# Kernel tuning notes

Measured on AMD Instinct MI355X. Metric: run time of the kernel, lower is better.

The kernel has to match this reference:

```python
import jax, jax.numpy as jnp
import numpy as np

B, N, C, NH = 8, 16384, 256, 8
CH = C // NH          # head dim = 32
SCALE = CH ** -0.5
HH = WW = 128         # N = HH*WW
# CoaT crpe window dict {3:2, 5:3, 7:3}: 2 heads->3x3, 3 heads->5x5, 3 heads->7x7


def setup_inputs() -> dict:
    key = jax.random.key(0)
    ks = jax.random.split(key, 9)
    w = lambda k, shp: (jax.random.normal(k, shp, jnp.float32) * 0.02)
    return {
        "x": jax.random.normal(ks[0], (B, N, C), jnp.float32),
        "w_qkv": w(ks[1], (C, 3 * C)),              # qkv_bias=False
        "w_proj": w(ks[2], (C, C)),
        "b_proj": jnp.zeros((C,), jnp.float32),
        "w3": w(ks[3], (3, 3, 1, 2 * CH)),          # HWIO depthwise, 2 heads
        "b3": jnp.zeros((2 * CH,), jnp.float32),
        "w5": w(ks[4], (5, 5, 1, 3 * CH)),          # 3 heads
        "b5": jnp.zeros((3 * CH,), jnp.float32),
        "w7": w(ks[5], (7, 7, 1, 3 * CH)),          # 3 heads
        "b7": jnp.zeros((3 * CH,), jnp.float32),
        "H": HH,
        "W": WW,
    }


def _hydra(q, k, v):
    # q,k,v: [B, h, N, Ch]; normalize over feature dim, O(N) token reduction
    qn = q * jax.lax.rsqrt(jnp.sum(q * q, axis=-1, keepdims=True))
    kn = k * jax.lax.rsqrt(jnp.sum(k * k, axis=-1, keepdims=True))
    kv = jnp.sum(kn * v, axis=-2, keepdims=True)   # [B, h, 1, Ch]
    return qn * kv                                  # broadcast over tokens


def _dwconv(img, kern, bias):
    # img: [B, c, H, W]; kern: [kh, kw, 1, c] (HWIO depthwise)
    c = img.shape[1]
    out = jax.lax.conv_general_dilated(
        img, kern, window_strides=(1, 1), padding="SAME",
        feature_group_count=c,
        dimension_numbers=("NCHW", "HWIO", "NCHW"))
    return out + bias[None, :, None, None]


def _crpe(q, v, Hs, Ws, convs):
    # CoaT ConvRelPosEnc: depthwise conv on v per head group, gated by q
    b, h, n, ch = v.shape
    outs, idx = [], 0
    for heads, kern, bias in convs:
        vs = v[:, idx:idx + heads]                          # [B, hs, N, Ch]
        v_img = vs.transpose(0, 1, 3, 2).reshape(b, heads * ch, Hs, Ws)
        cv = _dwconv(v_img, kern, bias)
        cv = cv.reshape(b, heads, ch, n).transpose(0, 1, 3, 2)
        outs.append(q[:, idx:idx + heads] * cv)
        idx += heads
    return jnp.concatenate(outs, axis=1)                    # [B, h, N, Ch]


def reference(x, w_qkv, w_proj, b_proj, w3, b3, w5, b5, w7, b7, H, W):
    b, n, c = x.shape
    qkv = (x @ w_qkv).reshape(b, n, 3, NH, CH).transpose(2, 0, 3, 1, 4)
    q, k, v = qkv[0], qkv[1], qkv[2]                        # [B, h, N, Ch]
    factor_att = _hydra(q, k, v)
    crpe = _crpe(q, v, H, W, [(2, w3, b3), (3, w5, b5), (3, w7, b7)])
    out = SCALE * factor_att + crpe
    out = out.transpose(0, 2, 1, 3).reshape(b, n, c)        # [B, N, C]
    return out @ w_proj + b_proj
```

## Files before the change

kernel.cpp:

```cpp
#include <hip/hip_runtime.h>
#include <hip/hip_bf16.h>


typedef __hip_bfloat16 bf16;
typedef __bf16 bf16x8 __attribute__((ext_vector_type(8)));
typedef unsigned short u16x8 __attribute__((ext_vector_type(8)));
typedef float f32x4 __attribute__((ext_vector_type(4)));
typedef float f32x8 __attribute__((ext_vector_type(8)));

#define SCALE_ 0.17677669529663687f

__device__ __forceinline__ unsigned short f2b(float f) {
  __hip_bfloat16 h = __float2bfloat16(f);
  return __builtin_bit_cast(unsigned short, h);
}
__device__ __forceinline__ float blo(unsigned u) {
  return __builtin_bit_cast(float, u << 16);
}
__device__ __forceinline__ float bhi(unsigned u) {
  return __builtin_bit_cast(float, u & 0xffff0000u);
}
__device__ __forceinline__ f32x8 unpack8(uint4 u) {
  f32x8 r;
  r[0] = blo(u.x); r[1] = bhi(u.x); r[2] = blo(u.y); r[3] = bhi(u.y);
  r[4] = blo(u.z); r[5] = bhi(u.z); r[6] = blo(u.w); r[7] = bhi(u.w);
  return r;
}
__device__ __forceinline__ uint4 pack8(float a0, float a1, float a2, float a3,
                                       float a4, float a5, float a6, float a7) {
  uint4 s;
  s.x = (unsigned)f2b(a0) | ((unsigned)f2b(a1) << 16);
  s.y = (unsigned)f2b(a2) | ((unsigned)f2b(a3) << 16);
  s.z = (unsigned)f2b(a4) | ((unsigned)f2b(a5) << 16);
  s.w = (unsigned)f2b(a6) | ((unsigned)f2b(a7) << 16);
  return s;
}
__device__ __forceinline__ void gload16(const void* g, void* l) {
  __builtin_amdgcn_global_load_lds(
      (const __attribute__((address_space(1))) unsigned int*)g,
      (__attribute__((address_space(3))) unsigned int*)l, 16, 0, 0);
}
__device__ __forceinline__ f32x4 mfma16(u16x8 a, u16x8 b, f32x4 c) {
  return __builtin_amdgcn_mfma_f32_16x16x32_bf16(
      __builtin_bit_cast(bf16x8, a), __builtin_bit_cast(bf16x8, b), c, 0, 0, 0);
}

__global__ __launch_bounds__(256) void prep_weights(
    const float* __restrict__ wqkv, const float* __restrict__ wproj,
    bf16* __restrict__ wqkvT, bf16* __restrict__ wprojT) {
  const int idx = blockIdx.x * 256 + threadIdx.x;
  if (idx < 768 * 256) {
    const int j = idx >> 8, k = idx & 255;
    wqkvT[idx] = __float2bfloat16(wqkv[k * 768 + j]);
  }
  if (idx < 256 * 256) {
    const int j = idx >> 8, k = idx & 255;
    wprojT[idx] = __float2bfloat16(wproj[k * 256 + j]);
  }
}

__global__ __launch_bounds__(256) void qkv_mfma(
    const float* __restrict__ x, const bf16* __restrict__ wT,
    bf16* __restrict__ qO, bf16* __restrict__ kO, bf16* __restrict__ vO) {
  __shared__ __align__(16) char LDSU[32768];
  char* As = LDSU;
  char* Bs = LDSU + 16384;
  const int tid = threadIdx.x;
  const int l = tid & 63, w = tid >> 6;
  const int wr = w >> 1, wc = w & 1;

  const int lin = blockIdx.y * 6 + blockIdx.x;
  const int xcd = lin & 7, qq = lin >> 3;
  const int jt = qq % 6;
  const int ttile = xcd * 128 + qq / 6;
  const int j0 = jt << 7;
  const int t0 = ttile << 7;

  f32x4 acc[4][4];
#pragma unroll
  for (int m = 0; m < 4; ++m)
#pragma unroll
    for (int t = 0; t < 4; ++t) acc[m][t] = (f32x4){0.f, 0.f, 0.f, 0.f};

  const int arow0 = w * 16 + (l >> 2), arow1 = arow0 + 64;
  const int asl = l & 3;
  const bf16* asrc0 =
      wT + (size_t)(j0 + arow0) * 256 + ((asl ^ ((arow0 >> 1) & 3)) << 3);
  const bf16* asrc1 =
      wT + (size_t)(j0 + arow1) * 256 + ((asl ^ ((arow1 >> 1) & 3)) << 3);
  const int ad0 = w * 1024;
  const int ad1 = 4096 + w * 1024;

  const int brow = tid >> 1, bkh = tid & 1;
  const float* xp = x + (size_t)(t0 + brow) * 256 + bkh * 16;
  const int bsw = (brow >> 1) & 3;
  const int bw0 = brow * 64 + (((bkh << 1) ^ bsw) << 4);
  const int bw1 = brow * 64 + ((((bkh << 1) | 1) ^ bsw) << 4);

  const int fr = l & 15;
  const int fq = l >> 4;
  const int fs = (fq ^ ((l >> 1) & 3)) << 4;

  {
    const float4 xa0 = *(const float4*)(xp);
    const float4 xa1 = *(const float4*)(xp + 4);
    const float4 xa2 = *(const float4*)(xp + 8);
    const float4 xa3 = *(const float4*)(xp + 12);
    gload16(asrc0, As + ad0);
    gload16(asrc1, As + ad1);
    u16x8 p0, p1;
    p0[0] = f2b(xa0.x); p0[1] = f2b(xa0.y); p0[2] = f2b(xa0.z); p0[3] = f2b(xa0.w);
    p0[4] = f2b(xa1.x); p0[5] = f2b(xa1.y); p0[6] = f2b(xa1.z); p0[7] = f2b(xa1.w);
    p1[0] = f2b(xa2.x); p1[1] = f2b(xa2.y); p1[2] = f2b(xa2.z); p1[3] = f2b(xa2.w);
    p1[4] = f2b(xa3.x); p1[5] = f2b(xa3.y); p1[6] = f2b(xa3.z); p1[7] = f2b(xa3.w);
    *(u16x8*)(Bs + bw0) = p0;
    *(u16x8*)(Bs + bw1) = p1;
  }
  __syncthreads();

  int cur = 0;
  for (int t = 0; t < 8; ++t) {
    const int kn = (t + 1) << 5;
    const int nxt = (cur ^ 1) << 13;
    float4 xa0, xa1, xa2, xa3;
    if (t < 7) {
      xa0 = *(const float4*)(xp + kn);
      xa1 = *(const float4*)(xp + kn + 4);
      xa2 = *(const float4*)(xp + kn + 8);
      xa3 = *(const float4*)(xp + kn + 12);
      gload16(asrc0 + kn, As + nxt + ad0);
      gload16(asrc1 + kn, As + nxt + ad1);
    }
    const char* Ac = As + (cur << 13);
    const char* Bc = Bs + (cur << 13);
    u16x8 af[4], bfv[4];
#pragma unroll
    for (int m = 0; m < 4; ++m)
      af[m] = *(const u16x8*)(Ac + (wr * 64 + m * 16 + fr) * 64 + fs);
#pragma unroll
    for (int tt = 0; tt < 4; ++tt)
      bfv[tt] = *(const u16x8*)(Bc + (wc * 64 + tt * 16 + fr) * 64 + fs);
#pragma unroll
    for (int m = 0; m < 4; ++m)
#pragma unroll
      for (int tt = 0; tt < 4; ++tt)
        acc[m][tt] = mfma16(af[m], bfv[tt], acc[m][tt]);
    if (t < 7) {
      u16x8 p0, p1;
      p0[0] = f2b(xa0.x); p0[1] = f2b(xa0.y); p0[2] = f2b(xa0.z); p0[3] = f2b(xa0.w);
      p0[4] = f2b(xa1.x); p0[5] = f2b(xa1.y); p0[6] = f2b(xa1.z); p0[7] = f2b(xa1.w);
      p1[0] = f2b(xa2.x); p1[1] = f2b(xa2.y); p1[2] = f2b(xa2.z); p1[3] = f2b(xa2.w);
      p1[4] = f2b(xa3.x); p1[5] = f2b(xa3.y); p1[6] = f2b(xa3.z); p1[7] = f2b(xa3.w);
      *(u16x8*)(Bs + nxt + bw0) = p0;
      *(u16x8*)(Bs + nxt + bw1) = p1;
    }
    __syncthreads();
    cur ^= 1;
  }

#pragma unroll
  for (int m = 0; m < 4; ++m) {
    const int jq = wr * 16 + m * 4 + fq;
#pragma unroll
    for (int t = 0; t < 4; ++t) {
      const int token = wc * 64 + t * 16 + fr;
      const int p = jq ^ (token & 15);
      uint2 pk;
      pk.x = (unsigned)f2b(acc[m][t][0]) | ((unsigned)f2b(acc[m][t][1]) << 16);
      pk.y = (unsigned)f2b(acc[m][t][2]) | ((unsigned)f2b(acc[m][t][3]) << 16);
      *(uint2*)(LDSU + token * 256 + (p << 3)) = pk;
    }
  }
  __syncthreads();

  const int region = j0 >> 8;
  bf16* outp = (region == 0) ? qO : ((region == 1) ? kO : vO);
  const int b = t0 >> 14;
  const int n0 = t0 & 16383;
  const int jl = j0 & 255;
  const int seg = tid & 15;
#pragma unroll
  for (int r = 0; r < 8; ++r) {
    const int token = r * 16 + (tid >> 4);
    const int tsw = token & 15;
    const int q0 = (2 * seg) ^ tsw;
    const int q1 = (2 * seg + 1) ^ tsw;
    const uint2 lo = *(const uint2*)(LDSU + token * 256 + (q0 << 3));
    const uint2 hi = *(const uint2*)(LDSU + token * 256 + (q1 << 3));
    uint4 d;
    d.x = lo.x; d.y = lo.y; d.z = hi.x; d.w = hi.y;
    *(uint4*)&outp[((size_t)b * 16384 + n0 + token) * 256 + jl + seg * 8] = d;
  }
}

__global__ __launch_bounds__(256) void kv_reduce(
    const bf16* __restrict__ kT, const bf16* __restrict__ vT,
    float* __restrict__ kv) {
  __shared__ float red[256 * 8];
  const int tid = threadIdx.x;
  const int b = blockIdx.y;
  const int seg = tid & 31;
  f32x8 part = (f32x8)0.f;

  for (int r = 0; r < 32; ++r) {
    const int token = blockIdx.x * 256 + r * 8 + (tid >> 5);
    const size_t roff = ((size_t)b * 16384 + token) * 256;
    const uint4 kd = *(const uint4*)(kT + roff + seg * 8);
    const f32x8 kf = unpack8(kd);
    float ss = 0.f;
#pragma unroll
    for (int i = 0; i < 8; ++i) ss += kf[i] * kf[i];
    ss += __shfl_xor(ss, 1);
    ss += __shfl_xor(ss, 2);
    const float inv = rsqrtf(ss);
    const uint4 vd = *(const uint4*)(vT + roff + seg * 8);
    const f32x8 vf = unpack8(vd);
#pragma unroll
    for (int i = 0; i < 8; ++i) part[i] += kf[i] * inv * vf[i];
  }
#pragma unroll
  for (int i = 0; i < 8; ++i) red[tid * 8 + i] = part[i];
  __syncthreads();
  if (tid < 32) {
    f32x8 s = (f32x8)0.f;
#pragma unroll
    for (int k = 0; k < 8; ++k)
#pragma unroll
      for (int i = 0; i < 8; ++i) s[i] += red[(tid + 32 * k) * 8 + i];
#pragma unroll
    for (int i = 0; i < 8; ++i)
      atomicAdd(&kv[b * 256 + seg * 8 + i], s[i]);
  }
}

template <int K>
__global__ __launch_bounds__(256) void crpe_conv(
    const bf16* __restrict__ qT, const bf16* __restrict__ vT,
    const float* __restrict__ kvbuf, const float* __restrict__ wp,
    const float* __restrict__ bp, int OC, int hbase,
    bf16* __restrict__ mid) {
  constexpr int R = K / 2;
  constexpr int S = 16 + 2 * R;
  constexpr int NSLOT = 4 * ((S - 1) * 23 + 1);
  __shared__ __align__(16) char vs[NSLOT * 16];
  __shared__ float wlds[K * K * 32];
  __shared__ float blds[32];

  const int tid = threadIdx.x;
  const int hg = blockIdx.x;
  const int h = hbase + hg;
  const int tile = blockIdx.y;
  const int b = blockIdx.z;
  const int tx0 = (tile & 7) * 16, ty0 = (tile >> 3) * 16;
  const int px = tid & 15, py = tid >> 4;
  const int ocbase = hg * 32;

  for (int e = tid; e < S * S; e += 256) {
    const int ly = e / S, lx = e - ly * S;
    const int gy = ty0 - R + ly, gx = tx0 - R + lx;
    uint4 d0 = {0, 0, 0, 0}, d1 = {0, 0, 0, 0}, d2 = {0, 0, 0, 0},
          d3 = {0, 0, 0, 0};
    if (gy >= 0 && gy < 128 && gx >= 0 && gx < 128) {
      const uint4* src = (const uint4*)(vT +
          ((size_t)b * 16384 + gy * 128 + gx) * 256 + h * 32);
      d0 = src[0]; d1 = src[1]; d2 = src[2]; d3 = src[3];
    }
    const int p = ly * 22 + lx;
    const int sw = (p >> 1) & 3;
    char* base = vs + ((p << 2) << 4);
    *(uint4*)(base + ((0 ^ sw) << 4)) = d0;
    *(uint4*)(base + ((1 ^ sw) << 4)) = d1;
    *(uint4*)(base + ((2 ^ sw) << 4)) = d2;
    *(uint4*)(base + ((3 ^ sw) << 4)) = d3;
  }
  for (int e = tid; e < K * K * 32; e += 256)
    wlds[e] = wp[(e >> 5) * OC + ocbase + (e & 31)];
  if (tid < 32) blds[tid] = bp[ocbase + tid];
  __syncthreads();

  const float4* bl4 = (const float4*)blds;
  f32x8 acc[4];
#pragma unroll
  for (int cc = 0; cc < 4; ++cc) {
    const float4 b0 = bl4[cc * 2], b1 = bl4[cc * 2 + 1];
    acc[cc][0] = b0.x; acc[cc][1] = b0.y; acc[cc][2] = b0.z; acc[cc][3] = b0.w;
    acc[cc][4] = b1.x; acc[cc][5] = b1.y; acc[cc][6] = b1.z; acc[cc][7] = b1.w;
  }
  const float4* wlds4 = (const float4*)wlds;
#pragma unroll 1
  for (int ky = 0; ky < K; ++ky) {
#pragma unroll
    for (int kx = 0; kx < K; ++kx) {
      const int p = (py + ky) * 22 + (px + kx);
      const int tap = ky * K + kx;
      const int sw = (p >> 1) & 3;
      const char* base = vs + ((p << 2) << 4);
#pragma unroll
      for (int cc = 0; cc < 4; ++cc) {
        const uint4 vv = *(const uint4*)(base + ((cc ^ sw) << 4));
        const f32x8 vf = unpack8(vv);
        const float4 w0 = wlds4[tap * 8 + cc * 2];
        const float4 w1 = wlds4[tap * 8 + cc * 2 + 1];
        acc[cc][0] += vf[0] * w0.x; acc[cc][1] += vf[1] * w0.y;
        acc[cc][2] += vf[2] * w0.z; acc[cc][3] += vf[3] * w0.w;
        acc[cc][4] += vf[4] * w1.x; acc[cc][5] += vf[5] * w1.y;
        acc[cc][6] += vf[6] * w1.z; acc[cc][7] += vf[7] * w1.w;
      }
    }
  }

  const int n = (ty0 + py) * 128 + (tx0 + px);
  const size_t off = ((size_t)b * 16384 + n) * 256 + h * 32;
  const uint4* qsrc = (const uint4*)(qT + off);
  f32x8 qv[4];
  float ss = 0.f;
#pragma unroll
  for (int cc = 0; cc < 4; ++cc) {
    qv[cc] = unpack8(qsrc[cc]);
#pragma unroll
    for (int i = 0; i < 8; ++i) ss += qv[cc][i] * qv[cc][i];
  }
  const float qinv = rsqrtf(ss);
  const float4* kvp = (const float4*)(kvbuf + ((size_t)b * 8 + h) * 32);
  uint4* mdst = (uint4*)(mid + off);
#pragma unroll
  for (int cc = 0; cc < 4; ++cc) {
    const float4 ka = kvp[cc * 2], kb = kvp[cc * 2 + 1];
    float o[8];
    o[0] = SCALE_ * qv[cc][0] * qinv * ka.x + qv[cc][0] * acc[cc][0];
    o[1] = SCALE_ * qv[cc][1] * qinv * ka.y + qv[cc][1] * acc[cc][1];
    o[2] = SCALE_ * qv[cc][2] * qinv * ka.z + qv[cc][2] * acc[cc][2];
    o[3] = SCALE_ * qv[cc][3] * qinv * ka.w + qv[cc][3] * acc[cc][3];
    o[4] = SCALE_ * qv[cc][4] * qinv * kb.x + qv[cc][4] * acc[cc][4];
    o[5] = SCALE_ * qv[cc][5] * qinv * kb.y + qv[cc][5] * acc[cc][5];
    o[6] = SCALE_ * qv[cc][6] * qinv * kb.z + qv[cc][6] * acc[cc][6];
    o[7] = SCALE_ * qv[cc][7] * qinv * kb.w + qv[cc][7] * acc[cc][7];
    mdst[cc] = pack8(o[0], o[1], o[2], o[3], o[4], o[5], o[6], o[7]);
  }
}

__global__ __launch_bounds__(256) void proj_mfma(
    const bf16* __restrict__ mid, const bf16* __restrict__ wpT,
    const float* __restrict__ bproj, float* __restrict__ out) {
  __shared__ __align__(16) char LDSU[32768];
  char* As = LDSU;
  char* Bs = LDSU + 16384;
  const int tid = threadIdx.x;
  const int l = tid & 63, w = tid >> 6;
  const int wr = w >> 1, wc = w & 1;

  const int lin = blockIdx.y * 2 + blockIdx.x;
  const int xcd = lin & 7, qq = lin >> 3;
  const int jt = qq & 1;
  const int ttile = xcd * 128 + (qq >> 1);
  const int j0 = jt << 7;
  const int tk0 = ttile << 7;

  f32x4 acc[4][4];
#pragma unroll
  for (int m = 0; m < 4; ++m)
#pragma unroll
    for (int t = 0; t < 4; ++t) acc[m][t] = (f32x4){0.f, 0.f, 0.f, 0.f};

  const int row0 = w * 16 + (l >> 2), row1 = row0 + 64;
  const int sl = l & 3;
  const int sw0 = (row0 >> 1) & 3, sw1 = (row1 >> 1) & 3;
  const bf16* asrc0 = wpT + (size_t)(j0 + row0) * 256 + ((sl ^ sw0) << 3);
  const bf16* asrc1 = wpT + (size_t)(j0 + row1) * 256 + ((sl ^ sw1) << 3);
  const bf16* bsrc0 = mid + (size_t)(tk0 + row0) * 256 + ((sl ^ sw0) << 3);
  const bf16* bsrc1 = mid + (size_t)(tk0 + row1) * 256 + ((sl ^ sw1) << 3);
  const int d0 = w * 1024;
  const int d1 = 4096 + w * 1024;

  const int fr = l & 15;
  const int fq = l >> 4;
  const int fs = (fq ^ ((l >> 1) & 3)) << 4;

  gload16(asrc0, As + d0);
  gload16(asrc1, As + d1);
  gload16(bsrc0, Bs + d0);
  gload16(bsrc1, Bs + d1);
  __syncthreads();

  int cur = 0;
  for (int t = 0; t < 8; ++t) {
    const int kn = (t + 1) << 5;
    const int nxt = (cur ^ 1) << 13;
    if (t < 7) {
      gload16(asrc0 + kn, As + nxt + d0);
      gload16(asrc1 + kn, As + nxt + d1);
      gload16(bsrc0 + kn, Bs + nxt + d0);
      gload16(bsrc1 + kn, Bs + nxt + d1);
    }
    const char* Ac = As + (cur << 13);
    const char* Bc = Bs + (cur << 13);
    u16x8 af[4], bfv[4];
#pragma unroll
    for (int m = 0; m < 4; ++m)
      af[m] = *(const u16x8*)(Ac + (wr * 64 + m * 16 + fr) * 64 + fs);
#pragma unroll
    for (int tt = 0; tt < 4; ++tt)
      bfv[tt] = *(const u16x8*)(Bc + (wc * 64 + tt * 16 + fr) * 64 + fs);
#pragma unroll
    for (int m = 0; m < 4; ++m)
#pragma unroll
      for (int tt = 0; tt < 4; ++tt)
        acc[m][tt] = mfma16(af[m], bfv[tt], acc[m][tt]);
    __syncthreads();
    cur ^= 1;
  }

#pragma unroll
  for (int m = 0; m < 4; ++m) {
    const float4 bias = *(const float4*)&bproj[j0 + wr * 64 + m * 16 + fq * 4];
#pragma unroll
    for (int t = 0; t < 4; ++t) {
      acc[m][t][0] += bias.x;
      acc[m][t][1] += bias.y;
      acc[m][t][2] += bias.z;
      acc[m][t][3] += bias.w;
    }
  }

  for (int chunk = 0; chunk < 2; ++chunk) {
    if (wc == chunk) {
#pragma unroll
      for (int m = 0; m < 4; ++m) {
        const int jq = wr * 16 + m * 4 + fq;
#pragma unroll
        for (int t = 0; t < 4; ++t) {
          const int ltok = t * 16 + fr;
          const int p = jq ^ (ltok & 15);
          float4 r;
          r.x = acc[m][t][0]; r.y = acc[m][t][1];
          r.z = acc[m][t][2]; r.w = acc[m][t][3];
          *(float4*)(LDSU + ltok * 512 + (p << 4)) = r;
        }
      }
    }
    __syncthreads();
    const int seg = tid & 31;
#pragma unroll
    for (int r = 0; r < 8; ++r) {
      const int ltok = r * 8 + (tid >> 5);
      const int p = seg ^ (ltok & 15);
      const float4 dv = *(const float4*)(LDSU + ltok * 512 + (p << 4));
      *(float4*)&out[(size_t)(tk0 + chunk * 64 + ltok) * 256 + j0 + seg * 4] = dv;
    }
    __syncthreads();
  }
}

extern "C" void kernel_launch(void* const* d_in, const int* in_sizes, int n_in,
                              void* d_out, int out_size, void* d_ws,
                              size_t ws_size, hipStream_t stream) {
  const float* x     = (const float*)d_in[0];
  const float* wqkv  = (const float*)d_in[1];
  const float* wproj = (const float*)d_in[2];
  const float* bproj = (const float*)d_in[3];
  const float* w3 = (const float*)d_in[4];
  const float* b3 = (const float*)d_in[5];
  const float* w5 = (const float*)d_in[6];
  const float* b5 = (const float*)d_in[7];
  const float* w7 = (const float*)d_in[8];
  const float* b7 = (const float*)d_in[9];
  float* out = (float*)d_out;

  const size_t PLANE = (size_t)8 * 16384 * 256;
  bf16* qT  = (bf16*)d_ws;
  bf16* vT  = qT + PLANE;
  bf16* kT  = vT + PLANE;
  bf16* mid = kT;
  float* kv = (float*)(kT + PLANE);
  bf16* wqkvT  = (bf16*)(kv + 2048);
  bf16* wprojT = wqkvT + 768 * 256;

  hipMemsetAsync(kv, 0, 2048 * sizeof(float), stream);
  prep_weights<<<dim3(768), 256, 0, stream>>>(wqkv, wproj, wqkvT, wprojT);
  qkv_mfma<<<dim3(6, 1024), 256, 0, stream>>>(x, wqkvT, qT, kT, vT);
  kv_reduce<<<dim3(64, 8), 256, 0, stream>>>(kT, vT, kv);
  crpe_conv<3><<<dim3(2, 64, 8), 256, 0, stream>>>(qT, vT, kv, w3, b3, 64, 0, mid);
  crpe_conv<5><<<dim3(3, 64, 8), 256, 0, stream>>>(qT, vT, kv, w5, b5, 96, 2, mid);
  crpe_conv<7><<<dim3(3, 64, 8), 256, 0, stream>>>(qT, vT, kv, w7, b7, 96, 5, mid);
  proj_mfma<<<dim3(2, 1024), 256, 0, stream>>>(mid, wprojT, bproj, out);
}
```

Measured before the change: 344.8 us.

## Keep full token tile resident in LDS and loop over all output column tiles

Both GEMM kernels now load a 128-token × 256 K activation tile once into LDS (converting x to bf16 in qkv) and loop over all output column tiles inside one block, streaming only the weight slices. This removes the 6× (qkv) and 2× (proj) re-reads and re-conversions of the activation rows across separate blocks. In exchange, each block uses 80 KB LDS, which lowers occupancy. The grid shrinks to 1024 blocks and the column loop runs serially, with extra syncs per tile.

```diff
diff --git a/kernel.cpp b/kernel.cpp
--- a/kernel.cpp
+++ b/kernel.cpp
@@ -62,134 +62,122 @@
 __global__ __launch_bounds__(256) void qkv_mfma(
     const float* __restrict__ x, const bf16* __restrict__ wT,
     bf16* __restrict__ qO, bf16* __restrict__ kO, bf16* __restrict__ vO) {
-  __shared__ __align__(16) char LDSU[32768];
-  char* As = LDSU;
-  char* Bs = LDSU + 16384;
+  __shared__ __align__(16) char XL[65536];
+  __shared__ __align__(16) char WB[16384];
   const int tid = threadIdx.x;
   const int l = tid & 63, w = tid >> 6;
   const int wr = w >> 1, wc = w & 1;
-
-  const int lin = blockIdx.y * 6 + blockIdx.x;
-  const int xcd = lin & 7, qq = lin >> 3;
-  const int jt = qq % 6;
-  const int ttile = xcd * 128 + qq / 6;
-  const int j0 = jt << 7;
-  const int t0 = ttile << 7;
-
-  f32x4 acc[4][4];
-#pragma unroll
-  for (int m = 0; m < 4; ++m)
-#pragma unroll
-    for (int t = 0; t < 4; ++t) acc[m][t] = (f32x4){0.f, 0.f, 0.f, 0.f};
+  const int t0 = (int)blockIdx.x << 7;
+  const int b = t0 >> 14;
+  const int n0 = t0 & 16383;
+
+  {
+    const int tk = tid >> 5;
+    const int s = tid & 31;
+    for (int r = 0; r < 16; ++r) {
+      const int row = r * 8 + tk;
+      const float4 a0 = *(const float4*)(x + (size_t)(t0 + row) * 256 + s * 8);
+      const float4 a1 =
+          *(const float4*)(x + (size_t)(t0 + row) * 256 + s * 8 + 4);
+      u16x8 p;
+      p[0] = f2b(a0.x); p[1] = f2b(a0.y); p[2] = f2b(a0.z); p[3] = f2b(a0.w);
+      p[4] = f2b(a1.x); p[5] = f2b(a1.y); p[6] = f2b(a1.z); p[7] = f2b(a1.w);
+      *(u16x8*)(XL + row * 512 + ((s ^ (row & 7)) << 4)) = p;
+    }
+  }
 
   const int arow0 = w * 16 + (l >> 2), arow1 = arow0 + 64;
   const int asl = l & 3;
-  const bf16* asrc0 =
-      wT + (size_t)(j0 + arow0) * 256 + ((asl ^ ((arow0 >> 1) & 3)) << 3);
-  const bf16* asrc1 =
-      wT + (size_t)(j0 + arow1) * 256 + ((asl ^ ((arow1 >> 1) & 3)) << 3);
-  const int ad0 = w * 1024;
-  const int ad1 = 4096 + w * 1024;
-
-  const int brow = tid >> 1, bkh = tid & 1;
-  const float* xp = x + (size_t)(t0 + brow) * 256 + bkh * 16;
-  const int bsw = (brow >> 1) & 3;
-  const int bw0 = brow * 64 + (((bkh << 1) ^ bsw) << 4);
-  const int bw1 = brow * 64 + ((((bkh << 1) | 1) ^ bsw) << 4);
+  const int aoff0 = ((asl ^ ((arow0 >> 1) & 3)) << 3);
+  const int aoff1 = ((asl ^ ((arow1 >> 1) & 3)) << 3);
+  const int ad0 = w * 1024, ad1 = 4096 + w * 1024;
 
   const int fr = l & 15;
   const int fq = l >> 4;
   const int fs = (fq ^ ((l >> 1) & 3)) << 4;
 
-  {
-    const float4 xa0 = *(const float4*)(xp);
-    const float4 xa1 = *(const float4*)(xp + 4);
-    const float4 xa2 = *(const float4*)(xp + 8);
-    const float4 xa3 = *(const float4*)(xp + 12);
-    gload16(asrc0, As + ad0);
-    gload16(asrc1, As + ad1);
-    u16x8 p0, p1;
-    p0[0] = f2b(xa0.x); p0[1] = f2b(xa0.y); p0[2] = f2b(xa0.z); p0[3] = f2b(xa0.w);
-    p0[4] = f2b(xa1.x); p0[5] = f2b(xa1.y); p0[6] = f2b(xa1.z); p0[7] = f2b(xa1.w);
-    p1[0] = f2b(xa2.x); p1[1] = f2b(xa2.y); p1[2] = f2b(xa2.z); p1[3] = f2b(xa2.w);
-    p1[4] = f2b(xa3.x); p1[5] = f2b(xa3.y); p1[6] = f2b(xa3.z); p1[7] = f2b(xa3.w);
-    *(u16x8*)(Bs + bw0) = p0;
-    *(u16x8*)(Bs + bw1) = p1;
-  }
-  __syncthreads();
-
-  int cur = 0;
-  for (int t = 0; t < 8; ++t) {
-    const int kn = (t + 1) << 5;
-    const int nxt = (cur ^ 1) << 13;
-    float4 xa0, xa1, xa2, xa3;
-    if (t < 7) {
-      xa0 = *(const float4*)(xp + kn);
-      xa1 = *(const float4*)(xp + kn + 4);
-      xa2 = *(const float4*)(xp + kn + 8);
-      xa3 = *(const float4*)(xp + kn + 12);
-      gload16(asrc0 + kn, As + nxt + ad0);
-      gload16(asrc1 + kn, As + nxt + ad1);
-    }
-    const char* Ac = As + (cur << 13);
-    const char* Bc = Bs + (cur << 13);
-    u16x8 af[4], bfv[4];
+  int btok[4], btsw[4];
+#pragma unroll
+  for (int tt = 0; tt < 4; ++tt) {
+    btok[tt] = wc * 64 + tt * 16 + fr;
+    btsw[tt] = btok[tt] & 7;
+  }
+
+#pragma unroll 1
+  for (int jt = 0; jt < 6; ++jt) {
+    const bf16* wbase = wT + (size_t)jt * 128 * 256;
+    f32x4 acc[4][4];
 #pragma unroll
     for (int m = 0; m < 4; ++m)
-      af[m] = *(const u16x8*)(Ac + (wr * 64 + m * 16 + fr) * 64 + fs);
-#pragma unroll
-    for (int tt = 0; tt < 4; ++tt)
-      bfv[tt] = *(const u16x8*)(Bc + (wc * 64 + tt * 16 + fr) * 64 + fs);
-#pragma unroll
-    for (int m = 0; m < 4; ++m)
+#pragma unroll
+      for (int t = 0; t < 4; ++t) acc[m][t] = (f32x4){0.f, 0.f, 0.f, 0.f};
+
+    gload16(wbase + (size_t)arow0 * 256 + aoff0, WB + ad0);
+    gload16(wbase + (size_t)arow1 * 256 + aoff1, WB + ad1);
+
+#pragma unroll 1
+    for (int t = 0; t < 8; ++t) {
+      __syncthreads();
+      if (t < 7) {
+        const int kn = (t + 1) * 32;
+        const int nb = ((t + 1) & 1) << 13;
+        gload16(wbase + (size_t)arow0 * 256 + kn + aoff0, WB + nb + ad0);
+        gload16(wbase + (size_t)arow1 * 256 + kn + aoff1, WB + nb + ad1);
+      }
+      const char* Ac = WB + ((t & 1) << 13);
+      u16x8 af[4], bfv[4];
+#pragma unroll
+      for (int m = 0; m < 4; ++m)
+        af[m] = *(const u16x8*)(Ac + (wr * 64 + m * 16 + fr) * 64 + fs);
 #pragma unroll
       for (int tt = 0; tt < 4; ++tt)
-        acc[m][tt] = mfma16(af[m], bfv[tt], acc[m][tt]);
-    if (t < 7) {
-      u16x8 p0, p1;
-      p0[0] = f2b(xa0.x); p0[1] = f2b(xa0.y); p0[2] = f2b(xa0.z); p0[3] = f2b(xa0.w);
-      p0[4] = f2b(xa1.x); p0[5] = f2b(xa1.y); p0[6] = f2b(xa1.z); p0[7] = f2b(xa1.w);
-      p1[0] = f2b(xa2.x); p1[1] = f2b(xa2.y); p1[2] = f2b(xa2.z); p1[3] = f2b(xa2.w);
-      p1[4] = f2b(xa3.x); p1[5] = f2b(xa3.y); p1[6] = f2b(xa3.z); p1[7] = f2b(xa3.w);
-      *(u16x8*)(Bs + nxt + bw0) = p0;
-      *(u16x8*)(Bs + nxt + bw1) = p1;
-    }
+        bfv[tt] = *(const u16x8*)(XL + btok[tt] * 512 +
+                                  (((4 * t + fq) ^ btsw[tt]) << 4));
+#pragma unroll
+      for (int m = 0; m < 4; ++m)
+#pragma unroll
+        for (int tt = 0; tt < 4; ++tt)
+          acc[m][tt] = mfma16(af[m], bfv[tt], acc[m][tt]);
+    }
+
+    const int region = jt >> 1;
+    bf16* outp = (region == 0) ? qO : ((region == 1) ? kO : vO);
+    const int jl = (jt & 1) * 128;
     __syncthreads();
-    cur ^= 1;
-  }
-
-#pragma unroll
-  for (int m = 0; m < 4; ++m) {
-    const int jq = wr * 16 + m * 4 + fq;
-#pragma unroll
-    for (int t = 0; t < 4; ++t) {
-      const int token = wc * 64 + t * 16 + fr;
-      const int p = jq ^ (token & 15);
-      uint2 pk;
-      pk.x = (unsigned)f2b(acc[m][t][0]) | ((unsigned)f2b(acc[m][t][1]) << 16);
-      pk.y = (unsigned)f2b(acc[m][t][2]) | ((unsigned)f2b(acc[m][t][3]) << 16);
-      *(uint2*)(LDSU + token * 256 + (p << 3)) = pk;
-    }
-  }
-  __syncthreads();
-
-  const int region = j0 >> 8;
-  bf16* outp = (region == 0) ? qO : ((region == 1) ? kO : vO);
-  const int b = t0 >> 14;
-  const int n0 = t0 & 16383;
-  const int jl = j0 & 255;
-  const int seg = tid & 15;
-#pragma unroll
-  for (int r = 0; r < 8; ++r) {
-    const int token = r * 16 + (tid >> 4);
-    const int tsw = token & 15;
-    const int q0 = (2 * seg) ^ tsw;
-    const int q1 = (2 * seg + 1) ^ tsw;
-    const uint2 lo = *(const uint2*)(LDSU + token * 256 + (q0 << 3));
-    const uint2 hi = *(const uint2*)(LDSU + token * 256 + (q1 << 3));
-    uint4 d;
-    d.x = lo.x; d.y = lo.y; d.z = hi.x; d.w = hi.y;
-    *(uint4*)&outp[((size_t)b * 16384 + n0 + token) * 256 + jl + seg * 8] = d;
+#pragma unroll 1
+    for (int c = 0; c < 2; ++c) {
+      if (wc == c) {
+#pragma unroll
+        for (int m = 0; m < 4; ++m) {
+          const int jq = wr * 16 + m * 4 + fq;
+#pragma unroll
+          for (int tt = 0; tt < 4; ++tt) {
+            const int ltok = tt * 16 + fr;
+            uint2 pk;
+            pk.x = (unsigned)f2b(acc[m][tt][0]) |
+                   ((unsigned)f2b(acc[m][tt][1]) << 16);
+            pk.y = (unsigned)f2b(acc[m][tt][2]) |
+                   ((unsigned)f2b(acc[m][tt][3]) << 16);
+            *(uint2*)(WB + ltok * 256 + ((jq ^ (ltok & 15)) << 3)) = pk;
+          }
+        }
+      }
+      __syncthreads();
+      const int seg = tid & 15;
+#pragma unroll
+      for (int r = 0; r < 4; ++r) {
+        const int ltok = r * 16 + (tid >> 4);
+        const int tsw = ltok & 15;
+        const uint2 lo = *(const uint2*)(WB + ltok * 256 + (((2 * seg) ^ tsw) << 3));
+        const uint2 hi =
+            *(const uint2*)(WB + ltok * 256 + (((2 * seg + 1) ^ tsw) << 3));
+        uint4 d;
+        d.x = lo.x; d.y = lo.y; d.z = hi.x; d.w = hi.y;
+        *(uint4*)&outp[((size_t)b * 16384 + n0 + c * 64 + ltok) * 256 + jl +
+                       seg * 8] = d;
+      }
+      __syncthreads();
+    }
   }
 }
 
@@ -342,112 +330,132 @@
 __global__ __launch_bounds__(256) void proj_mfma(
     const bf16* __restrict__ mid, const bf16* __restrict__ wpT,
     const float* __restrict__ bproj, float* __restrict__ out) {
-  __shared__ __align__(16) char LDSU[32768];
-  char* As = LDSU;
-  char* Bs = LDSU + 16384;
+  __shared__ __align__(16) char XL[65536];
+  __shared__ __align__(16) char WB[16384];
   const int tid = threadIdx.x;
   const int l = tid & 63, w = tid >> 6;
   const int wr = w >> 1, wc = w & 1;
-
-  const int lin = blockIdx.y * 2 + blockIdx.x;
-  const int xcd = lin & 7, qq = lin >> 3;
-  const int jt = qq & 1;
-  const int ttile = xcd * 128 + (qq >> 1);
-  const int j0 = jt << 7;
-  const int tk0 = ttile << 7;
-
-  f32x4 acc[4][4];
-#pragma unroll
-  for (int m = 0; m < 4; ++m)
-#pragma unroll
-    for (int t = 0; t < 4; ++t) acc[m][t] = (f32x4){0.f, 0.f, 0.f, 0.f};
-
-  const int row0 = w * 16 + (l >> 2), row1 = row0 + 64;
-  const int sl = l & 3;
-  const int sw0 = (row0 >> 1) & 3, sw1 = (row1 >> 1) & 3;
-  const bf16* asrc0 = wpT + (size_t)(j0 + row0) * 256 + ((sl ^ sw0) << 3);
-  const bf16* asrc1 = wpT + (size_t)(j0 + row1) * 256 + ((sl ^ sw1) << 3);
-  const bf16* bsrc0 = mid + (size_t)(tk0 + row0) * 256 + ((sl ^ sw0) << 3);
-  const bf16* bsrc1 = mid + (size_t)(tk0 + row1) * 256 + ((sl ^ sw1) << 3);
-  const int d0 = w * 1024;
-  const int d1 = 4096 + w * 1024;
+  const int t0 = (int)blockIdx.x << 7;
+  const int b = t0 >> 14;
+  const int n0 = t0 & 16383;
+
+  {
+    const int ltk = l >> 5;
+    const int s = l & 31;
+#pragma unroll 1
+    for (int i = 0; i < 16; ++i) {
+      const int shot_tok = w * 32 + i * 2;
+      const int tok = shot_tok + ltk;
+      gload16(mid + ((size_t)b * 16384 + n0 + tok) * 256 +
+                  ((s ^ (tok & 7)) << 3),
+              XL + shot_tok * 512);
+    }
+  }
+
+  const int arow0 = w * 16 + (l >> 2), arow1 = arow0 + 64;
+  const int asl = l & 3;
+  const int aoff0 = ((asl ^ ((arow0 >> 1) & 3)) << 3);
+  const int aoff1 = ((asl ^ ((arow1 >> 1) & 3)) << 3);
+  const int ad0 = w * 1024, ad1 = 4096 + w * 1024;
 
   const int fr = l & 15;
   const int fq = l >> 4;
   const int fs = (fq ^ ((l >> 1) & 3)) << 4;
 
-  gload16(asrc0, As + d0);
-  gload16(asrc1, As + d1);
-  gload16(bsrc0, Bs + d0);
-  gload16(bsrc1, Bs + d1);
-  __syncthreads();
-
-  int cur = 0;
-  for (int t = 0; t < 8; ++t) {
-    const int kn = (t + 1) << 5;
-    const int nxt = (cur ^ 1) << 13;
-    if (t < 7) {
-      gload16(asrc0 + kn, As + nxt + d0);
-      gload16(asrc1 + kn, As + nxt + d1);
-      gload16(bsrc0 + kn, Bs + nxt + d0);
-      gload16(bsrc1 + kn, Bs + nxt + d1);
-    }
-    const char* Ac = As + (cur << 13);
-    const char* Bc = Bs + (cur << 13);
-    u16x8 af[4], bfv[4];
+  int btok[4], btsw[4];
+#pragma unroll
+  for (int tt = 0; tt < 4; ++tt) {
+    btok[tt] = wc * 64 + tt * 16 + fr;
+    btsw[tt] = btok[tt] & 7;
+  }
+
+#pragma unroll 1
+  for (int jt = 0; jt < 2; ++jt) {
+    const bf16* wbase = wpT + (size_t)jt * 128 * 256;
+    const int j0 = jt * 128;
+    f32x4 acc[4][4];
 #pragma unroll
     for (int m = 0; m < 4; ++m)
-      af[m] = *(const u16x8*)(Ac + (wr * 64 + m * 16 + fr) * 64 + fs);
-#pragma unroll
-    for (int tt = 0; tt < 4; ++tt)
-      bfv[tt] = *(const u16x8*)(Bc + (wc * 64 + tt * 16 + fr) * 64 + fs);
-#pragma unroll
-    for (int m = 0; m < 4; ++m)
+#pragma unroll
+      for (int t = 0; t < 4; ++t) acc[m][t] = (f32x4){0.f, 0.f, 0.f, 0.f};
+
+    gload16(wbase + (size_t)arow0 * 256 + aoff0, WB + ad0);
+    gload16(wbase + (size_t)arow1 * 256 + aoff1, WB + ad1);
+
+#pragma unroll 1
+    for (int t = 0; t < 8; ++t) {
+      __syncthreads();
+      if (t < 7) {
+        const int kn = (t + 1) * 32;
+        const int nb = ((t + 1) & 1) << 13;
+        gload16(wbase + (size_t)arow0 * 256 + kn + aoff0, WB + nb + ad0);
+        gload16(wbase + (size_t)arow1 * 256 + kn + aoff1, WB + nb + ad1);
+      }
+      const char* Ac = WB + ((t & 1) << 13);
+      u16x8 af[4], bfv[4];
+#pragma unroll
+      for (int m = 0; m < 4; ++m)
+        af[m] = *(const u16x8*)(Ac + (wr * 64 + m * 16 + fr) * 64 + fs);
 #pragma unroll
       for (int tt = 0; tt < 4; ++tt)
-        acc[m][tt] = mfma16(af[m], bfv[tt], acc[m][tt]);
+        bfv[tt] = *(const u16x8*)(XL + btok[tt] * 512 +
+                                  (((4 * t + fq) ^ btsw[tt]) << 4));
+#pragma unroll
+      for (int m = 0; m < 4; ++m)
+#pragma unroll
+        for (int tt = 0; tt < 4; ++tt)
+          acc[m][tt] = mfma16(af[m], bfv[tt], acc[m][tt]);
+    }
+
+#pragma unroll
+    for (int m = 0; m < 4; ++m) {
+      const float4 bias =
+          *(const float4*)&bproj[j0 + wr * 64 + m * 16 + fq * 4];
+#pragma unroll
+      for (int t = 0; t < 4; ++t) {
+        acc[m][t][0] += bias.x;
+        acc[m][t][1] += bias.y;
+        acc[m][t][2] += bias.z;
+        acc[m][t][3] += bias.w;
+      }
+    }
+
     __syncthreads();
-    cur ^= 1;
-  }
-
-#pragma unroll
-  for (int m = 0; m < 4; ++m) {
-    const float4 bias = *(const float4*)&bproj[j0 + wr * 64 + m * 16 + fq * 4];
-#pragma unroll
-    for (int t = 0; t < 4; ++t) {
-      acc[m][t][0] += bias.x;
-      acc[m][t][1] += bias.y;
-      acc[m][t][2] += bias.z;
-      acc[m][t][3] += bias.w;
-    }
-  }
-
-  for (int chunk = 0; chunk < 2; ++chunk) {
-    if (wc == chunk) {
-#pragma unroll
-      for (int m = 0; m < 4; ++m) {
-        const int jq = wr * 16 + m * 4 + fq;
-#pragma unroll
-        for (int t = 0; t < 4; ++t) {
-          const int ltok = t * 16 + fr;
-          const int p = jq ^ (ltok & 15);
-          float4 r;
-          r.x = acc[m][t][0]; r.y = acc[m][t][1];
-          r.z = acc[m][t][2]; r.w = acc[m][t][3];
-          *(float4*)(LDSU + ltok * 512 + (p << 4)) = r;
+#pragma unroll 1
+    for (int r = 0; r < 4; ++r) {
+      if (wc == (r >> 1)) {
+        const int tb = (r & 1) * 2;
+#pragma unroll
+        for (int m = 0; m < 4; ++m) {
+          const int sq = wr * 16 + m * 4 + fq;
+#pragma unroll
+          for (int ti = 0; ti < 2; ++ti) {
+            const int tt = tb + ti;
+            const int ltok = ti * 16 + fr;
+            float4 rv;
+            rv.x = acc[m][tt][0]; rv.y = acc[m][tt][1];
+            rv.z = acc[m][tt][2]; rv.w = acc[m][tt][3];
+            *(float4*)(WB + ltok * 512 + ((sq ^ (ltok & 7)) << 4)) = rv;
+          }
         }
       }
-    }
-    __syncthreads();
-    const int seg = tid & 31;
-#pragma unroll
-    for (int r = 0; r < 8; ++r) {
-      const int ltok = r * 8 + (tid >> 5);
-      const int p = seg ^ (ltok & 15);
-      const float4 dv = *(const float4*)(LDSU + ltok * 512 + (p << 4));
-      *(float4*)&out[(size_t)(tk0 + chunk * 64 + ltok) * 256 + j0 + seg * 4] = dv;
-    }
-    __syncthreads();
+      __syncthreads();
+#pragma unroll
+      for (int i = 0; i < 2; ++i) {
+        const int lin = i * 256 + tid;
+        const int ltok = lin >> 5, seg = lin & 31;
+        const float4 dv =
+            *(const float4*)(WB + ltok * 512 + ((seg ^ (ltok & 7)) << 4));
+        *(float4*)&out[(size_t)(t0 + r * 32 + ltok) * 256 + j0 + seg * 4] = dv;
+        const int lin2 = lin + 512;
+        const int ltok2 = lin2 >> 5, seg2 = lin2 & 31;
+        const float4 dv2 =
+            *(const float4*)(WB + ltok2 * 512 + ((seg2 ^ (ltok2 & 7)) << 4));
+        *(float4*)&out[(size_t)(t0 + r * 32 + ltok2) * 256 + j0 + seg2 * 4] =
+            dv2;
+      }
+      __syncthreads();
+    }
   }
 }
 
@@ -477,10 +485,10 @@
 
   hipMemsetAsync(kv, 0, 2048 * sizeof(float), stream);
   prep_weights<<<dim3(768), 256, 0, stream>>>(wqkv, wproj, wqkvT, wprojT);
-  qkv_mfma<<<dim3(6, 1024), 256, 0, stream>>>(x, wqkvT, qT, kT, vT);
+  qkv_mfma<<<dim3(1024), 256, 0, stream>>>(x, wqkvT, qT, kT, vT);
   kv_reduce<<<dim3(64, 8), 256, 0, stream>>>(kT, vT, kv);
   crpe_conv<3><<<dim3(2, 64, 8), 256, 0, stream>>>(qT, vT, kv, w3, b3, 64, 0, mid);
   crpe_conv<5><<<dim3(3, 64, 8), 256, 0, stream>>>(qT, vT, kv, w5, b5, 96, 2, mid);
   crpe_conv<7><<<dim3(3, 64, 8), 256, 0, stream>>>(qT, vT, kv, w7, b7, 96, 5, mid);
-  proj_mfma<<<dim3(2, 1024), 256, 0, stream>>>(mid, wprojT, bproj, out);
-}
+  proj_mfma<<<dim3(1024), 256, 0, stream>>>(mid, wprojT, bproj, out);
+}
```

After: 487.2 us. 1.41x slower.

## Deepen GEMM prefetch pipelines with partial-wait barriers and merge crpe conv launches

Applied to the files above, without the earlier changes.

The qkv GEMM now keeps three stages of x register prefetch in flight. The proj GEMM uses a triple-buffered LDS ring with loads issued two stages ahead. In both, full __syncthreads is replaced by s_waitcnt vmcnt(N) barriers and MFMA sections are raised with s_setprio, so global loads can overlap compute instead of draining every iteration. The three crpe conv kernels become one launch that dispatches on head index, removing two launches and the tail idle between them. Costs are more registers, more LDS in proj (48KB, which may lower occupancy) and hand-counted vmcnt values that must match the exact number of outstanding loads.

```diff
diff --git a/kernel.cpp b/kernel.cpp
--- a/kernel.cpp
+++ b/kernel.cpp
@@ -43,6 +43,21 @@
 __device__ __forceinline__ f32x4 mfma16(u16x8 a, u16x8 b, f32x4 c) {
   return __builtin_amdgcn_mfma_f32_16x16x32_bf16(
       __builtin_bit_cast(bf16x8, a), __builtin_bit_cast(bf16x8, b), c, 0, 0, 0);
+}
+__device__ __forceinline__ void barrier_vm4() {
+  asm volatile("s_waitcnt vmcnt(4) lgkmcnt(0)" ::: "memory");
+  __builtin_amdgcn_s_barrier();
+  asm volatile("" ::: "memory");
+}
+__device__ __forceinline__ void barrier_vm0() {
+  asm volatile("s_waitcnt vmcnt(0) lgkmcnt(0)" ::: "memory");
+  __builtin_amdgcn_s_barrier();
+  asm volatile("" ::: "memory");
+}
+__device__ __forceinline__ void barrier_vm8() {
+  asm volatile("s_waitcnt vmcnt(8) lgkmcnt(0)" ::: "memory");
+  __builtin_amdgcn_s_barrier();
+  asm volatile("" ::: "memory");
 }
 
 __global__ __launch_bounds__(256) void prep_weights(
@@ -88,8 +103,7 @@
       wT + (size_t)(j0 + arow0) * 256 + ((asl ^ ((arow0 >> 1) & 3)) << 3);
   const bf16* asrc1 =
       wT + (size_t)(j0 + arow1) * 256 + ((asl ^ ((arow1 >> 1) & 3)) << 3);
-  const int ad0 = w * 1024;
-  const int ad1 = 4096 + w * 1024;
+  const int ad0 = w * 1024, ad1 = 4096 + w * 1024;
 
   const int brow = tid >> 1, bkh = tid & 1;
   const float* xp = x + (size_t)(t0 + brow) * 256 + bkh * 16;
@@ -101,38 +115,45 @@
   const int fq = l >> 4;
   const int fs = (fq ^ ((l >> 1) & 3)) << 4;
 
+  float4 xs[3][4];
+
+  gload16(asrc0, As + ad0);
+  gload16(asrc1, As + ad1);
+#pragma unroll
+  for (int s = 0; s < 3; ++s)
+#pragma unroll
+    for (int i = 0; i < 4; ++i)
+      xs[s][i] = *(const float4*)(xp + s * 32 + i * 4);
   {
-    const float4 xa0 = *(const float4*)(xp);
-    const float4 xa1 = *(const float4*)(xp + 4);
-    const float4 xa2 = *(const float4*)(xp + 8);
-    const float4 xa3 = *(const float4*)(xp + 12);
-    gload16(asrc0, As + ad0);
-    gload16(asrc1, As + ad1);
     u16x8 p0, p1;
-    p0[0] = f2b(xa0.x); p0[1] = f2b(xa0.y); p0[2] = f2b(xa0.z); p0[3] = f2b(xa0.w);
-    p0[4] = f2b(xa1.x); p0[5] = f2b(xa1.y); p0[6] = f2b(xa1.z); p0[7] = f2b(xa1.w);
-    p1[0] = f2b(xa2.x); p1[1] = f2b(xa2.y); p1[2] = f2b(xa2.z); p1[3] = f2b(xa2.w);
-    p1[4] = f2b(xa3.x); p1[5] = f2b(xa3.y); p1[6] = f2b(xa3.z); p1[7] = f2b(xa3.w);
+    p0[0] = f2b(xs[0][0].x); p0[1] = f2b(xs[0][0].y);
+    p0[2] = f2b(xs[0][0].z); p0[3] = f2b(xs[0][0].w);
+    p0[4] = f2b(xs[0][1].x); p0[5] = f2b(xs[0][1].y);
+    p0[6] = f2b(xs[0][1].z); p0[7] = f2b(xs[0][1].w);
+    p1[0] = f2b(xs[0][2].x); p1[1] = f2b(xs[0][2].y);
+    p1[2] = f2b(xs[0][2].z); p1[3] = f2b(xs[0][2].w);
+    p1[4] = f2b(xs[0][3].x); p1[5] = f2b(xs[0][3].y);
+    p1[6] = f2b(xs[0][3].z); p1[7] = f2b(xs[0][3].w);
     *(u16x8*)(Bs + bw0) = p0;
     *(u16x8*)(Bs + bw1) = p1;
   }
-  __syncthreads();
-
-  int cur = 0;
+  barrier_vm8();
+
+#pragma unroll
   for (int t = 0; t < 8; ++t) {
-    const int kn = (t + 1) << 5;
-    const int nxt = (cur ^ 1) << 13;
-    float4 xa0, xa1, xa2, xa3;
     if (t < 7) {
-      xa0 = *(const float4*)(xp + kn);
-      xa1 = *(const float4*)(xp + kn + 4);
-      xa2 = *(const float4*)(xp + kn + 8);
-      xa3 = *(const float4*)(xp + kn + 12);
-      gload16(asrc0 + kn, As + nxt + ad0);
-      gload16(asrc1 + kn, As + nxt + ad1);
-    }
-    const char* Ac = As + (cur << 13);
-    const char* Bc = Bs + (cur << 13);
+      const int kn = (t + 1) << 5;
+      char* Adst = As + (((t + 1) & 1) << 13);
+      gload16(asrc0 + kn, Adst + ad0);
+      gload16(asrc1 + kn, Adst + ad1);
+    }
+    if (t < 5) {
+#pragma unroll
+      for (int i = 0; i < 4; ++i)
+        xs[t % 3][i] = *(const float4*)(xp + (t + 3) * 32 + i * 4);
+    }
+    const char* Ac = As + ((t & 1) << 13);
+    const char* Bc = Bs + ((t & 1) << 13);
     u16x8 af[4], bfv[4];
 #pragma unroll
     for (int m = 0; m < 4; ++m)
@@ -140,23 +161,32 @@
 #pragma unroll
     for (int tt = 0; tt < 4; ++tt)
       bfv[tt] = *(const u16x8*)(Bc + (wc * 64 + tt * 16 + fr) * 64 + fs);
+    __builtin_amdgcn_s_setprio(1);
 #pragma unroll
     for (int m = 0; m < 4; ++m)
 #pragma unroll
       for (int tt = 0; tt < 4; ++tt)
         acc[m][tt] = mfma16(af[m], bfv[tt], acc[m][tt]);
+    __builtin_amdgcn_s_setprio(0);
     if (t < 7) {
+      const float4* xv = xs[(t + 1) % 3];
       u16x8 p0, p1;
-      p0[0] = f2b(xa0.x); p0[1] = f2b(xa0.y); p0[2] = f2b(xa0.z); p0[3] = f2b(xa0.w);
-      p0[4] = f2b(xa1.x); p0[5] = f2b(xa1.y); p0[6] = f2b(xa1.z); p0[7] = f2b(xa1.w);
-      p1[0] = f2b(xa2.x); p1[1] = f2b(xa2.y); p1[2] = f2b(xa2.z); p1[3] = f2b(xa2.w);
-      p1[4] = f2b(xa3.x); p1[5] = f2b(xa3.y); p1[6] = f2b(xa3.z); p1[7] = f2b(xa3.w);
-      *(u16x8*)(Bs + nxt + bw0) = p0;
-      *(u16x8*)(Bs + nxt + bw1) = p1;
-    }
-    __syncthreads();
-    cur ^= 1;
-  }
+      p0[0] = f2b(xv[0].x); p0[1] = f2b(xv[0].y);
+      p0[2] = f2b(xv[0].z); p0[3] = f2b(xv[0].w);
+      p0[4] = f2b(xv[1].x); p0[5] = f2b(xv[1].y);
+      p0[6] = f2b(xv[1].z); p0[7] = f2b(xv[1].w);
+      p1[0] = f2b(xv[2].x); p1[1] = f2b(xv[2].y);
+      p1[2] = f2b(xv[2].z); p1[3] = f2b(xv[2].w);
+      p1[4] = f2b(xv[3].x); p1[5] = f2b(xv[3].y);
+      p1[6] = f2b(xv[3].z); p1[7] = f2b(xv[3].w);
+      char* Bdst = Bs + (((t + 1) & 1) << 13);
+      *(u16x8*)(Bdst + bw0) = p0;
+      *(u16x8*)(Bdst + bw1) = p1;
+    }
+    if (t < 5) barrier_vm4();
+    else if (t < 7) barrier_vm0();
+  }
+  __syncthreads();
 
 #pragma unroll
   for (int m = 0; m < 4; ++m) {
@@ -183,10 +213,9 @@
   for (int r = 0; r < 8; ++r) {
     const int token = r * 16 + (tid >> 4);
     const int tsw = token & 15;
-    const int q0 = (2 * seg) ^ tsw;
-    const int q1 = (2 * seg + 1) ^ tsw;
-    const uint2 lo = *(const uint2*)(LDSU + token * 256 + (q0 << 3));
-    const uint2 hi = *(const uint2*)(LDSU + token * 256 + (q1 << 3));
+    const uint2 lo = *(const uint2*)(LDSU + token * 256 + (((2 * seg) ^ tsw) << 3));
+    const uint2 hi =
+        *(const uint2*)(LDSU + token * 256 + (((2 * seg + 1) ^ tsw) << 3));
     uint4 d;
     d.x = lo.x; d.y = lo.y; d.z = hi.x; d.w = hi.y;
     *(uint4*)&outp[((size_t)b * 16384 + n0 + token) * 256 + jl + seg * 8] = d;
@@ -233,22 +262,22 @@
   }
 }
 
+#define CRPE_SMEM 37632
+
 template <int K>
-__global__ __launch_bounds__(256) void crpe_conv(
-    const bf16* __restrict__ qT, const bf16* __restrict__ vT,
+__device__ __forceinline__ void crpe_impl(
+    char* smem, const bf16* __restrict__ qT, const bf16* __restrict__ vT,
     const float* __restrict__ kvbuf, const float* __restrict__ wp,
-    const float* __restrict__ bp, int OC, int hbase,
+    const float* __restrict__ bp, int OC, int hg, int h,
     bf16* __restrict__ mid) {
   constexpr int R = K / 2;
   constexpr int S = 16 + 2 * R;
   constexpr int NSLOT = 4 * ((S - 1) * 23 + 1);
-  __shared__ __align__(16) char vs[NSLOT * 16];
-  __shared__ float wlds[K * K * 32];
-  __shared__ float blds[32];
+  char* vs = smem;
+  float* wlds = (float*)(smem + NSLOT * 16);
+  float* blds = wlds + K * K * 32;
 
   const int tid = threadIdx.x;
-  const int hg = blockIdx.x;
-  const int h = hbase + hg;
   const int tile = blockIdx.y;
   const int b = blockIdx.z;
   const int tx0 = (tile & 7) * 16, ty0 = (tile >> 3) * 16;
@@ -339,12 +368,29 @@
   }
 }
 
+__global__ __launch_bounds__(256) void crpe_all(
+    const bf16* __restrict__ qT, const bf16* __restrict__ vT,
+    const float* __restrict__ kvbuf,
+    const float* __restrict__ w3, const float* __restrict__ b3,
+    const float* __restrict__ w5, const float* __restrict__ b5,
+    const float* __restrict__ w7, const float* __restrict__ b7,
+    bf16* __restrict__ mid) {
+  __shared__ __align__(16) char smem[CRPE_SMEM];
+  const int h = blockIdx.x;
+  if (h < 2)
+    crpe_impl<3>(smem, qT, vT, kvbuf, w3, b3, 64, h, h, mid);
+  else if (h < 5)
+    crpe_impl<5>(smem, qT, vT, kvbuf, w5, b5, 96, h - 2, h, mid);
+  else
+    crpe_impl<7>(smem, qT, vT, kvbuf, w7, b7, 96, h - 5, h, mid);
+}
+
 __global__ __launch_bounds__(256) void proj_mfma(
     const bf16* __restrict__ mid, const bf16* __restrict__ wpT,
     const float* __restrict__ bproj, float* __restrict__ out) {
-  __shared__ __align__(16) char LDSU[32768];
+  __shared__ __align__(16) char LDSU[49152];
   char* As = LDSU;
-  char* Bs = LDSU + 16384;
+  char* Bs = LDSU + 24576;
   const int tid = threadIdx.x;
   const int l = tid & 63, w = tid >> 6;
   const int wr = w >> 1, wc = w & 1;
@@ -369,8 +415,7 @@
   const bf16* asrc1 = wpT + (size_t)(j0 + row1) * 256 + ((sl ^ sw1) << 3);
   const bf16* bsrc0 = mid + (size_t)(tk0 + row0) * 256 + ((sl ^ sw0) << 3);
   const bf16* bsrc1 = mid + (size_t)(tk0 + row1) * 256 + ((sl ^ sw1) << 3);
-  const int d0 = w * 1024;
-  const int d1 = 4096 + w * 1024;
+  const int d0 = w * 1024, d1 = 4096 + w * 1024;
 
   const int fr = l & 15;
   const int fq = l >> 4;
@@ -380,20 +425,24 @@
   gload16(asrc1, As + d1);
   gload16(bsrc0, Bs + d0);
   gload16(bsrc1, Bs + d1);
-  __syncthreads();
-
-  int cur = 0;
+  gload16(asrc0 + 32, As + 8192 + d0);
+  gload16(asrc1 + 32, As + 8192 + d1);
+  gload16(bsrc0 + 32, Bs + 8192 + d0);
+  gload16(bsrc1 + 32, Bs + 8192 + d1);
+  barrier_vm4();
+
+#pragma unroll
   for (int t = 0; t < 8; ++t) {
-    const int kn = (t + 1) << 5;
-    const int nxt = (cur ^ 1) << 13;
-    if (t < 7) {
-      gload16(asrc0 + kn, As + nxt + d0);
-      gload16(asrc1 + kn, As + nxt + d1);
-      gload16(bsrc0 + kn, Bs + nxt + d0);
-      gload16(bsrc1 + kn, Bs + nxt + d1);
-    }
-    const char* Ac = As + (cur << 13);
-    const char* Bc = Bs + (cur << 13);
+    if (t < 6) {
+      const int kn = (t + 2) << 5;
+      const int nb = ((t + 2) % 3) * 8192;
+      gload16(asrc0 + kn, As + nb + d0);
+      gload16(asrc1 + kn, As + nb + d1);
+      gload16(bsrc0 + kn, Bs + nb + d0);
+      gload16(bsrc1 + kn, Bs + nb + d1);
+    }
+    const char* Ac = As + (t % 3) * 8192;
+    const char* Bc = Bs + (t % 3) * 8192;
     u16x8 af[4], bfv[4];
 #pragma unroll
     for (int m = 0; m < 4; ++m)
@@ -401,14 +450,17 @@
 #pragma unroll
     for (int tt = 0; tt < 4; ++tt)
       bfv[tt] = *(const u16x8*)(Bc + (wc * 64 + tt * 16 + fr) * 64 + fs);
+    __builtin_amdgcn_s_setprio(1);
 #pragma unroll
     for (int m = 0; m < 4; ++m)
 #pragma unroll
       for (int tt = 0; tt < 4; ++tt)
         acc[m][tt] = mfma16(af[m], bfv[tt], acc[m][tt]);
-    __syncthreads();
-    cur ^= 1;
-  }
+    __builtin_amdgcn_s_setprio(0);
+    if (t < 6) barrier_vm4();
+    else if (t < 7) barrier_vm0();
+  }
+  __syncthreads();
 
 #pragma unroll
   for (int m = 0; m < 4; ++m) {
@@ -479,8 +531,7 @@
   prep_weights<<<dim3(768), 256, 0, stream>>>(wqkv, wproj, wqkvT, wprojT);
   qkv_mfma<<<dim3(6, 1024), 256, 0, stream>>>(x, wqkvT, qT, kT, vT);
   kv_reduce<<<dim3(64, 8), 256, 0, stream>>>(kT, vT, kv);
-  crpe_conv<3><<<dim3(2, 64, 8), 256, 0, stream>>>(qT, vT, kv, w3, b3, 64, 0, mid);
-  crpe_conv<5><<<dim3(3, 64, 8), 256, 0, stream>>>(qT, vT, kv, w5, b5, 96, 2, mid);
-  crpe_conv<7><<<dim3(3, 64, 8), 256, 0, stream>>>(qT, vT, kv, w7, b7, 96, 5, mid);
+  crpe_all<<<dim3(8, 64, 8), 256, 0, stream>>>(qT, vT, kv, w3, b3, w5, b5, w7,
+                                               b7, mid);
   proj_mfma<<<dim3(2, 1024), 256, 0, stream>>>(mid, wprojT, bproj, out);
 }
```

Measured after the change: 373.5 us. +8.3%, slower.
